# Performance work log

Hardware: AMD Instinct MI355X
Metric: run time of the kernel (lower is better)

Reference implementation:

```python
import jax, jax.numpy as jnp
import numpy as np

B, N, D, H = 4, 2048, 1024, 16
HD = D // H
LR_SCALE = 0.01  # base step size for the fast-weight test-time update
EPS = 1e-6


def setup_inputs() -> dict:
    key = jax.random.key(0)
    ks = jax.random.split(key, 11)
    s = 0.02
    x = jax.random.normal(ks[0], (B, N, D), jnp.float32)
    Wq = jax.random.normal(ks[1], (D, D), jnp.float32) * s
    Wk = jax.random.normal(ks[2], (D, D), jnp.float32) * s
    Wv = jax.random.normal(ks[3], (D, D), jnp.float32) * s
    Wo = jax.random.normal(ks[4], (D, D), jnp.float32) * s
    w1_init = jax.random.normal(ks[5], (H, HD, HD), jnp.float32) * s  # FastWeightGLU init state
    w3_init = jax.random.normal(ks[6], (H, HD, HD), jnp.float32) * s
    W_lr = jax.random.normal(ks[7], (D, H), jnp.float32) * s  # FastWeightHpGLU lr head
    norm_w = jnp.ones((D,), jnp.float32)  # grouped RMSNorm weight
    Wg1 = jax.random.normal(ks[8], (D, HD), jnp.float32) * s  # output_gate bottleneck
    Wg2 = jax.random.normal(ks[9], (HD, D), jnp.float32) * s
    return dict(x=x, Wq=Wq, Wk=Wk, Wv=Wv, Wo=Wo, w1_init=w1_init,
                w3_init=w3_init, W_lr=W_lr, norm_w=norm_w, Wg1=Wg1, Wg2=Wg2)


def _fast_weight_train(q, k, v, lr, w1_init, w3_init):
    # q,k,v: (b,n,h,hd); lr: (b,n,h); fast weight f(x) = silu(x@W1) * (x@W3)
    b = q.shape[0]
    W1_0 = jnp.broadcast_to(w1_init, (b,) + w1_init.shape)
    W3_0 = jnp.broadcast_to(w3_init, (b,) + w3_init.shape)

    def step(carry, inp):
        W1, W3 = carry
        q_t, k_t, v_t, lr_t = inp  # (b,h,hd), lr_t: (b,h,1)
        h1 = jnp.einsum('bhd,bhde->bhe', k_t, W1)
        h3 = jnp.einsum('bhd,bhde->bhe', k_t, W3)
        sg = jax.nn.sigmoid(h1)
        s1 = h1 * sg  # silu(h1)
        err = s1 * h3 - v_t  # d(0.5||f(k)-v||^2)/df
        dsilu = sg * (1.0 + h1 * (1.0 - sg))
        g1 = err * h3 * dsilu
        g3 = err * s1
        W1 = W1 - lr_t[..., None] * jnp.einsum('bhd,bhe->bhde', k_t, g1)
        W3 = W3 - lr_t[..., None] * jnp.einsum('bhd,bhe->bhde', k_t, g3)
        o1 = jnp.einsum('bhd,bhde->bhe', q_t, W1)
        o3 = jnp.einsum('bhd,bhde->bhe', q_t, W3)
        return (W1, W3), jax.nn.silu(o1) * o3

    xs = (q.transpose(1, 0, 2, 3), k.transpose(1, 0, 2, 3),
          v.transpose(1, 0, 2, 3), lr.transpose(1, 0, 2)[..., None])
    (W1, W3), outs = jax.lax.scan(step, (W1_0, W3_0), xs)
    return outs.transpose(1, 0, 2, 3), (W1, W3)  # (b,n,h,hd)


def reference(x, Wq, Wk, Wv, Wo, w1_init, w3_init, W_lr, norm_w, Wg1, Wg2):
    b, n, d = x.shape
    h = w1_init.shape[0]
    hd = d // h
    q = jax.nn.silu((x @ Wq).reshape(b, n, h, hd))
    k = jax.nn.silu((x @ Wk).reshape(b, n, h, hd))
    v = (x @ Wv).reshape(b, n, h, hd)
    lr = LR_SCALE * jax.nn.sigmoid(x @ W_lr)  # (b,n,h) per-token hyper-param
    out, _ = _fast_weight_train(q, k, v, lr, w1_init, w3_init)
    # grouped RMSNorm (per head) fused with sigmoid output gate
    rms = jax.lax.rsqrt(jnp.mean(out * out, axis=-1, keepdims=True) + EPS)
    out = (out * rms).reshape(b, n, d) * norm_w
    gate = (x @ Wg1) @ Wg2
    out = out * jax.nn.sigmoid(gate)
    return out @ Wo
```

## Files before the change

kernel.cpp:

```cpp
#include <hip/hip_runtime.h>
#include <hip/hip_bf16.h>

#define B_ 4
#define N_ 2048
#define D_ 1024
#define H_ 16
#define HD_ 64
#define MTOT (B_*N_)
#define CH_ 16
#define NCH_ (N_/CH_)

typedef __attribute__((ext_vector_type(8))) short short8v;
typedef __attribute__((ext_vector_type(4))) float f32x4;

__device__ __forceinline__ float fsig(float x){
  return __builtin_amdgcn_rcpf(1.0f + __expf(-x));
}

__global__ void k_cast_bf16(const float* __restrict__ in, __hip_bfloat16* __restrict__ out, int n4){
  int i = blockIdx.x*256 + threadIdx.x;
  if (i >= n4) return;
  float4 vv = ((const float4*)in)[i];
  __hip_bfloat16 b0 = __float2bfloat16(vv.x), b1 = __float2bfloat16(vv.y),
                 b2 = __float2bfloat16(vv.z), b3 = __float2bfloat16(vv.w);
  ushort4 o;
  o.x = *(const unsigned short*)&b0; o.y = *(const unsigned short*)&b1;
  o.z = *(const unsigned short*)&b2; o.w = *(const unsigned short*)&b3;
  ((ushort4*)out)[i] = o;
}

__global__ void k_transpose_cast(const float* __restrict__ in, __hip_bfloat16* __restrict__ out,
                                 int R, int C){
  __shared__ float tile[64][65];
  int r0 = blockIdx.y*64, c0 = blockIdx.x*64;
  int tid = threadIdx.x;
  #pragma unroll
  for (int i=0;i<16;i++){ int idx = tid + i*256; int rr = idx>>6, cc = idx&63;
    tile[rr][cc] = in[(size_t)(r0+rr)*C + (c0+cc)]; }
  __syncthreads();
  #pragma unroll
  for (int i=0;i<16;i++){ int idx = tid + i*256; int rr = idx>>6, cc = idx&63;
    out[(size_t)(c0+rr)*R + (r0+cc)] = __float2bfloat16(tile[cc][rr]); }
// ... 46 lines not shown
  short* lA = As + wid*1024;
  short* lB = Bs + wid*1024;
  const int row = lane & 15, kq = (lane >> 4)*8;
  for (int kk = 0; kk < K; kk += 32) {
    __syncthreads();
    gl2lds16(Aps + aoff0 + kk,                 lA);
    gl2lds16(Aps + aoff0 + (size_t)16*K + kk,  lA + 512);
    gl2lds16(Bps + boff0 + kk,                 lB);
    gl2lds16(Bps + boff0 + (size_t)16*K + kk,  lB + 512);
    __syncthreads();
    short8v af[4], bfr[4];
    #pragma unroll
    for (int i=0;i<4;i++) af[i]  = *(const short8v*)(As + (wm*64 + i*16 + row)*32 + kq);
    #pragma unroll
    for (int j=0;j<4;j++) bfr[j] = *(const short8v*)(Bs + (wn*64 + j*16 + row)*32 + kq);
    #pragma unroll
    for (int i=0;i<4;i++)
      #pragma unroll
      for (int j=0;j<4;j++)
        acc[i][j] = __builtin_amdgcn_mfma_f32_16x16x32_bf16(af[i], bfr[j], acc[i][j], 0, 0, 0);
  }
  #pragma unroll
  for (int i=0;i<4;i++){
    #pragma unroll
    for (int j=0;j<4;j++){
      int col = n0 + wn*64 + j*16 + (lane & 15);
      #pragma unroll
      for (int qq=0; qq<4; ++qq){
        int rowg = m0 + wm*64 + i*16 + (lane>>4)*4 + qq;
        float val = acc[i][j][qq];
        if (LAYOUT==0) {
          if (ACT==1) val = val*fsig(val);
          C[(size_t)rowg*N + col] = val;
        } else if (LAYOUT==1) {
          if (ACT==1) val = val*fsig(val);
          size_t oidx = ((((size_t)(rowg>>11))*16 + (col>>6))*(size_t)N_ + (size_t)(rowg & 2047))*64
                        + (size_t)(col & 63);
          C[oidx] = val;
        } else {
          const int t3 = col >> 10, cc2 = col & 1023;
          if (t3 < 2) val = val*fsig(val);
          size_t oidx = (size_t)t3*((size_t)MTOT*D_)
                      + ((((size_t)(rowg>>11))*16 + (cc2>>6))*(size_t)N_ + (size_t)(rowg & 2047))*64
                      + (size_t)(cc2 & 63);
          C[oidx] = val;
        }
      }
    }
  }
}

__device__ __forceinline__ unsigned short bfr16(float x){
  __hip_bfloat16 b = __float2bfloat16(x);
  return *(unsigned short*)&b;
}
__device__ __forceinline__ short8v cvt_frag(const float4 a, const float4 c){
  short8v r;
  r[0]=(short)bfr16(a.x); r[1]=(short)bfr16(a.y); r[2]=(short)bfr16(a.z); r[3]=(short)bfr16(a.w);
  r[4]=(short)bfr16(c.x); r[5]=(short)bfr16(c.y); r[6]=(short)bfr16(c.z); r[7]=(short)bfr16(c.w);
  return r;
}

__global__ __launch_bounds__(256,1) void k_scan8(
    const float* __restrict__ q, const float* __restrict__ k, const float* __restrict__ v,
    const float* __restrict__ lr, const float* __restrict__ w1i, const float* __restrict__ w3i,
    float* __restrict__ so)
{
  const int blk = blockIdx.x;
  const int bh  = blk >> 2;
  const int sl  = blk & 3;
  const int b = bh >> 4, h = bh & 15;
  const int e0 = sl*16;
  const int tid = threadIdx.x, lane = tid & 63, wid = tid >> 6;
  const int tA = lane & 15, ks8 = (lane >> 4)*8;

  __shared__ __align__(16) __hip_bfloat16 Wb1[16*64];
  __shared__ __align__(16) __hip_bfloat16 Wb3[16*64];
  __shared__ __align__(16) float KW1e[256], KW3e[256];
  __shared__ __align__(16) float QW1[256], QW3[256];
  __shared__ __align__(16) float GKK[256], GQK[256];
  __shared__ __align__(16) float C13[512];
  __shared__ __align__(16) float kS[16][68];

  const int we = tid & 15;
  const int wd = (tid >> 4) * 4;
  float w1r[4], w3r[4];
  {
    const float* w1p = w1i + (size_t)h*HD_*HD_ + e0 + we;
    const float* w3p = w3i + (size_t)h*HD_*HD_ + e0 + we;
    #pragma unroll
    for (int j=0;j<4;j++){ w1r[j] = w1p[(size_t)(wd+j)*64]; w3r[j] = w3p[(size_t)(wd+j)*64]; }
  }
  const int mir_off = we*128 + ((wd*2) ^ ((we&7)<<4));
  auto write_mirrors = [&](){
    uint2 p1, p3;
    p1.x = (unsigned)bfr16(w1r[0]) | ((unsigned)bfr16(w1r[1])<<16);
    p1.y = (unsigned)bfr16(w1r[2]) | ((unsigned)bfr16(w1r[3])<<16);
    p3.x = (unsigned)bfr16(w3r[0]) | ((unsigned)bfr16(w3r[1])<<16);
    p3.y = (unsigned)bfr16(w3r[2]) | ((unsigned)bfr16(w3r[3])<<16);
    *(uint2*)((char*)Wb1 + mir_off) = p1;
    *(uint2*)((char*)Wb3 + mir_off) = p3;
  };
  write_mirrors();

  const float* kfb = k + (size_t)bh*N_*64;
  const float* qfb = q + (size_t)bh*N_*64;
  const float* vfb = v + (size_t)bh*N_*64;
  const float* lrp = lr + ((size_t)b*N_)*16 + h;
  float* sob = so + (((size_t)b*N_)*16 + h)*64 + e0;

  auto mir_read = [&](const __hip_bfloat16* Wm, int m)->short8v{
    return *(const short8v*)((const char*)Wm + tA*128 + (((m*32+ks8)*2) ^ ((tA&7)<<4)));
  };

  float4 fA0,fA1,fA2,fA3;
  float4 fB0,fB1,fB2,fB3;
  float  vvr[16], lrr[16];

  if (wid >= 1) {
    const float* xr = ((wid==2) ? qfb : kfb) + (size_t)tA*64;
    fA0 = *(const float4*)(xr+ks8);    fA1 = *(const float4*)(xr+ks8+4);
    fA2 = *(const float4*)(xr+32+ks8); fA3 = *(const float4*)(xr+32+ks8+4);
    if (wid==3){
      const float* qr = qfb + (size_t)tA*64;
      fB0 = *(const float4*)(qr+ks8);    fB1 = *(const float4*)(qr+ks8+4);
      fB2 = *(const float4*)(qr+32+ks8); fB3 = *(const float4*)(qr+32+ks8+4);
    }
  } else if (lane < 16) {
    #pragma unroll
    for (int t=0;t<CH_;++t){
      vvr[t] = vfb[(size_t)t*64 + e0 + lane];
      lrr[t] = lrp[(size_t)t*16];
    }
  }
  __syncthreads();

  #pragma unroll 1
  for (int c = 0; c < NCH_; ++c) {
    const int t0 = c*CH_;

    if (wid == 1) {
      *(float4*)&kS[tA][ks8]      = fA0;
      *(float4*)&kS[tA][ks8+4]    = fA1;
      *(float4*)&kS[tA][32+ks8]   = fA2;
      *(float4*)&kS[tA][32+ks8+4] = fA3;
      short8v af0 = cvt_frag(fA0,fA1), af1 = cvt_frag(fA2,fA3);
      const int slot = (((lane>>4)*4) ^ ((( tA>>1)&3)<<2));
      f32x4 acc = {};
      acc = __builtin_amdgcn_mfma_f32_16x16x32_bf16(af0, mir_read(Wb1,0), acc, 0,0,0);
      acc = __builtin_amdgcn_mfma_f32_16x16x32_bf16(af1, mir_read(Wb1,1), acc, 0,0,0);
      *(f32x4*)&KW1e[tA*16 + slot] = acc;
      f32x4 ac3 = {};
      ac3 = __builtin_amdgcn_mfma_f32_16x16x32_bf16(af0, mir_read(Wb3,0), ac3, 0,0,0);
      ac3 = __builtin_amdgcn_mfma_f32_16x16x32_bf16(af1, mir_read(Wb3,1), ac3, 0,0,0);
      *(f32x4*)&KW3e[tA*16 + slot] = ac3;
    } else if (wid == 2) {
      short8v af0 = cvt_frag(fA0,fA1), af1 = cvt_frag(fA2,fA3);
      f32x4 acc = {};
      acc = __builtin_amdgcn_mfma_f32_16x16x32_bf16(af0, mir_read(Wb1,0), acc, 0,0,0);
      acc = __builtin_amdgcn_mfma_f32_16x16x32_bf16(af1, mir_read(Wb1,1), acc, 0,0,0);
      #pragma unroll
      for (int qq=0;qq<4;++qq) QW1[((lane>>4)*4+qq)*16 + tA] = acc[qq];
      f32x4 ac3 = {};
      ac3 = __builtin_amdgcn_mfma_f32_16x16x32_bf16(af0, mir_read(Wb3,0), ac3, 0,0,0);
      ac3 = __builtin_amdgcn_mfma_f32_16x16x32_bf16(af1, mir_read(Wb3,1), ac3, 0,0,0);
      #pragma unroll
      for (int qq=0;qq<4;++qq) QW3[((lane>>4)*4+qq)*16 + tA] = ac3[qq];
    } else if (wid == 3) {
      short8v af0 = cvt_frag(fA0,fA1), af1 = cvt_frag(fA2,fA3);
      short8v aq0 = cvt_frag(fB0,fB1), aq1 = cvt_frag(fB2,fB3);
      f32x4 acc = {};
      acc = __builtin_amdgcn_mfma_f32_16x16x32_bf16(af0, af0, acc, 0,0,0);
      acc = __builtin_amdgcn_mfma_f32_16x16x32_bf16(af1, af1, acc, 0,0,0);
      #pragma unroll
      for (int qq=0;qq<4;++qq) GKK[((lane>>4)*4+qq)*16 + tA] = acc[qq];
      f32x4 ac2 = {};
      ac2 = __builtin_amdgcn_mfma_f32_16x16x32_bf16(aq0, af0, ac2, 0,0,0);
      ac2 = __builtin_amdgcn_mfma_f32_16x16x32_bf16(aq1, af1, ac2, 0,0,0);
      #pragma unroll
      for (int qq=0;qq<4;++qq) GQK[((lane>>4)*4+qq)*16 + tA] = ac2[qq];
    }
    __syncthreads();

    const int tn0 = ((c+1 < NCH_) ? c+1 : c) * CH_;
    if (wid >= 1) {
      const float* xr = ((wid==2) ? qfb : kfb) + (size_t)(tn0+tA)*64;
      fA0 = *(const float4*)(xr+ks8);    fA1 = *(const float4*)(xr+ks8+4);
      fA2 = *(const float4*)(xr+32+ks8); fA3 = *(const float4*)(xr+32+ks8+4);
      if (wid==3){
        const float* qr = qfb + (size_t)(tn0+tA)*64;
        fB0 = *(const float4*)(qr+ks8);    fB1 = *(const float4*)(qr+ks8+4);
        fB2 = *(const float4*)(qr+32+ks8); fB3 = *(const float4*)(qr+32+ks8+4);
      }
    } else if (lane < 16) {
      float vvn[16], lrn[16];
      #pragma unroll
      for (int t=0;t<CH_;++t){
        vvn[t] = vfb[(size_t)(tn0+t)*64 + e0 + lane];
        lrn[t] = lrp[(size_t)(tn0+t)*16];
      }
      float a1[16], a3[16];
      const int swr = ((lane>>1)&3)<<2;
      #pragma unroll
      for (int i2=0;i2<4;i2++){
        f32x4 x1 = *(const f32x4*)&KW1e[lane*16 + ((i2*4) ^ swr)];
        f32x4 x3 = *(const f32x4*)&KW3e[lane*16 + ((i2*4) ^ swr)];
        a1[i2*4+0]=x1[0]; a1[i2*4+1]=x1[1]; a1[i2*4+2]=x1[2]; a1[i2*4+3]=x1[3];
        a3[i2*4+0]=x3[0]; a3[i2*4+1]=x3[1]; a3[i2*4+2]=x3[2]; a3[i2*4+3]=x3[3];
      }
      f32x4 grow[3][4];
      #pragma unroll
      for (int i2=0;i2<4;i2++){
        grow[0][i2] = *(const f32x4*)&GKK[ 0 + i2*4];
        grow[1][i2] = *(const f32x4*)&GKK[16 + i2*4];
        grow[2][i2] = *(const f32x4*)&GKK[32 + i2*4];
      }
      #pragma unroll
      for (int t = 0; t < CH_; ++t) {
        const float h1 = a1[t], h3 = a3[t];
        const float sg = fsig(h1);
        const float s1 = h1*sg;
        const float er = fmaf(s1, h3, -vvr[t]);
        const float ds = sg*fmaf(h1, 1.0f - sg, 1.0f);
        const float lt = lrr[t];
        float2 cc; cc.x = lt*(er*h3*ds); cc.y = lt*(er*s1);
        *(float2*)&C13[(t*16+lane)*2] = cc;
        #pragma unroll
        for (int t2 = t+1; t2 < CH_; ++t2) {
          const float g = grow[t%3][t2>>2][t2&3];
          a1[t2] = fmaf(-g, cc.x, a1[t2]);
          a3[t2] = fmaf(-g, cc.y, a3[t2]);
        }
        if (t + 3 < CH_) {
          #pragma unroll
          for (int i2=0;i2<4;i2++) grow[(t+3)%3][i2] = *(const f32x4*)&GKK[(t+3)*16 + i2*4];
        }
      }
      #pragma unroll
      for (int t=0;t<CH_;++t){ vvr[t]=vvn[t]; lrr[t]=lrn[t]; }
    }
    __syncthreads();

    {
      const int ot = tid >> 4, oe = tid & 15;
      float o1 = QW1[ot*16+oe], o3 = QW3[ot*16+oe];
      #pragma unroll
      for (int s = 0; s < CH_; ++s) {
        const float gl2 = GQK[ot*16+s];
        const float2 cc = *(const float2*)&C13[(s*16+oe)*2];
        const float g = (s <= ot) ? gl2 : 0.0f;
        o1 = fmaf(-g, cc.x, o1);
        o3 = fmaf(-g, cc.y, o3);
      }
      sob[(size_t)(t0+ot)*(H_*HD_) + oe] = (o1*fsig(o1))*o3;
    }

    #pragma unroll
    for (int s = 0; s < CH_; ++s) {
      const float2 cc = *(const float2*)&C13[(s*16+we)*2];
      const float4 ks = *(const float4*)&kS[s][wd];
      w1r[0] = fmaf(-ks.x, cc.x, w1r[0]); w1r[1] = fmaf(-ks.y, cc.x, w1r[1]);
      w1r[2] = fmaf(-ks.z, cc.x, w1r[2]); w1r[3] = fmaf(-ks.w, cc.x, w1r[3]);
      w3r[0] = fmaf(-ks.x, cc.y, w3r[0]); w3r[1] = fmaf(-ks.y, cc.y, w3r[1]);
      w3r[2] = fmaf(-ks.z, cc.y, w3r[2]); w3r[3] = fmaf(-ks.w, cc.y, w3r[3]);
    }
    write_mirrors();
    __syncthreads();
  }
}

__global__ void k_norm_gate(const float* __restrict__ so, const float* __restrict__ gate,
                            const float* __restrict__ nw, __hip_bfloat16* __restrict__ y)
{
  int idx = blockIdx.x*4 + (threadIdx.x>>6);
  int e = threadIdx.x & 63;
  float o = so[(size_t)idx*64 + e];
  float ss = o*o;
  #pragma unroll
  for (int m=32; m>=1; m>>=1) ss += __shfl_xor(ss, m, 64);
  float rms = rsqrtf(ss*(1.0f/64.0f) + 1e-6f);
  int hh = idx & 15;
  size_t bn = (size_t)(idx >> 4);
  int d = hh*64 + e;
  float g = gate[bn*1024 + d];
  float val = o*rms*nw[d] * fsig(g);
  y[bn*1024 + d] = __float2bfloat16(val);
}

extern "C" void kernel_launch(void* const* d_in, const int* in_sizes, int n_in,
                              void* d_out, int out_size, void* d_ws, size_t ws_size,
                              hipStream_t stream)
{
  const float* x   = (const float*)d_in[0];
  const float* Wq  = (const float*)d_in[1];
  const float* Wk  = (const float*)d_in[2];
  const float* Wv  = (const float*)d_in[3];
  const float* Wo  = (const float*)d_in[4];
  const float* w1i = (const float*)d_in[5];
  const float* w3i = (const float*)d_in[6];
  const float* Wlr = (const float*)d_in[7];
  const float* nw  = (const float*)d_in[8];
  const float* Wg1 = (const float*)d_in[9];
  const float* Wg2 = (const float*)d_in[10];
  float* out = (float*)d_out;

  char* p = (char*)d_ws;
  auto take = [&](size_t bytes)->void*{ void* r = (void*)p; p += (bytes + 255) & ~(size_t)255; return r; };
  __hip_bfloat16* xb    = (__hip_bfloat16*)take((size_t)MTOT*D_*2);
  __hip_bfloat16* WqkvT = (__hip_bfloat16*)take((size_t)3*D_*D_*2);
  __hip_bfloat16* Wot   = (__hip_bfloat16*)take((size_t)D_*D_*2);
  __hip_bfloat16* Wg2t  = (__hip_bfloat16*)take((size_t)D_*HD_*2);
  __hip_bfloat16* WgL   = (__hip_bfloat16*)take((size_t)128*D_*2);
  __hip_bfloat16* t1b   = (__hip_bfloat16*)take((size_t)MTOT*HD_*2);
  float* projt = (float*)take((size_t)MTOT*128*4);
  float* qf  = (float*)take((size_t)MTOT*D_*4);
  float* kf  = (float*)take((size_t)MTOT*D_*4);
  float* vf  = (float*)take((size_t)MTOT*D_*4);
  float* lrb = (float*)take((size_t)MTOT*H_*4);
  float* sob = (float*)take((size_t)MTOT*D_*4);
  __hip_bfloat16* yb = (__hip_bfloat16*)take((size_t)MTOT*D_*2);
  (void)kf; (void)vf;

  k_cast_bf16<<<MTOT*D_/4/256, 256, 0, stream>>>(x, xb, MTOT*D_/4);
  k_transpose_cast<<<dim3(16,16), 256, 0, stream>>>(Wq, WqkvT,             D_, D_);
  k_transpose_cast<<<dim3(16,16), 256, 0, stream>>>(Wk, WqkvT + D_*D_,     D_, D_);
  k_transpose_cast<<<dim3(16,16), 256, 0, stream>>>(Wv, WqkvT + 2*D_*D_,   D_, D_);
  k_transpose_cast<<<dim3(16,16), 256, 0, stream>>>(Wo, Wot, D_, D_);
  k_transpose_cast<<<dim3(16,1),  256, 0, stream>>>(Wg2, Wg2t, HD_, D_);
  k_prep_wgl<<<512, 256, 0, stream>>>(Wg1, Wlr, WgL);
  k_gemm_bt2<0,0><<<dim3(1,64), 256, 0, stream>>>(xb, WgL, projt, MTOT, 128, D_);
  k_post_gl<<<MTOT/4, 256, 0, stream>>>(projt, t1b, lrb);
  k_gemm_bt2<1,2><<<dim3(24,64), 256, 0, stream>>>(xb, WqkvT, qf, MTOT, 3*D_, D_);
  k_gemm_bt2<0,0><<<dim3(8,64), 256, 0, stream>>>(t1b, Wg2t, out, MTOT, D_, HD_);
  k_scan8<<<256, 256, 0, stream>>>(qf, kf, vf, lrb, w1i, w3i, sob);
  k_norm_gate<<<MTOT*H_/4, 256, 0, stream>>>(sob, out, nw, yb);
  k_gemm_bt2<0,0><<<dim3(8,64), 256, 0, stream>>>(yb, Wot, out, MTOT, D_, D_);
}
```

Measured before the change: 524.6 us.

## Double scan chunk size to 32 tokens and stage v/lr through shared memory

Raises the chunked fast-weight scan from 16 to 32 tokens per chunk, halving the number of serial chunk iterations and barriers, and extends the MFMA Gram/projection tiles to 32x32. v and lr prefetch moves from wave 0's registers to waves 1-3, which write them into shared memory after each chunk. The serial in-chunk recurrence on wave 0 grows quadratically with chunk size (32x32 triangle), and register pressure rises, which may offset the reduction in sync overhead.

```diff
diff --git a/kernel.cpp b/kernel.cpp
--- a/kernel.cpp
+++ b/kernel.cpp
@@ -7,7 +7,7 @@
 #define H_ 16
 #define HD_ 64
 #define MTOT (B_*N_)
-#define CH_ 16
+#define CH_ 32
 #define NCH_ (N_/CH_)
 
 typedef __attribute__((ext_vector_type(8))) short short8v;
@@ -149,7 +149,7 @@
   return r;
 }
 
-__global__ __launch_bounds__(256,1) void k_scan8(
+__global__ __launch_bounds__(256,1) void k_scan12(
     const float* __restrict__ q, const float* __restrict__ k, const float* __restrict__ v,
     const float* __restrict__ lr, const float* __restrict__ w1i, const float* __restrict__ w3i,
     float* __restrict__ so)
@@ -160,15 +160,18 @@
   const int b = bh >> 4, h = bh & 15;
   const int e0 = sl*16;
   const int tid = threadIdx.x, lane = tid & 63, wid = tid >> 6;
-  const int tA = lane & 15, ks8 = (lane >> 4)*8;
+  const int tA = lane & 15, g = lane >> 4;
+  const int ks8 = g*8;
 
   __shared__ __align__(16) __hip_bfloat16 Wb1[16*64];
   __shared__ __align__(16) __hip_bfloat16 Wb3[16*64];
-  __shared__ __align__(16) float KW1e[256], KW3e[256];
-  __shared__ __align__(16) float QW1[256], QW3[256];
-  __shared__ __align__(16) float GKK[256], GQK[256];
-  __shared__ __align__(16) float C13[512];
-  __shared__ __align__(16) float kS[16][68];
+  __shared__ __align__(16) float KW1e[16*32], KW3e[16*32];
+  __shared__ __align__(16) float QW1[32*16], QW3[32*16];
+  __shared__ __align__(16) float GKK[32*32], GQK[32*32];
+  __shared__ __align__(16) float C13[32*16*2];
+  __shared__ __align__(16) float kS[32][68];
+  __shared__ __align__(16) float vS[32*16];
+  __shared__ float lrS[32];
 
   const int we = tid & 15;
   const int wd = (tid >> 4) * 4;
@@ -201,26 +204,59 @@
     return *(const short8v*)((const char*)Wm + tA*128 + (((m*32+ks8)*2) ^ ((tA&7)<<4)));
   };
 
-  float4 fA0,fA1,fA2,fA3;
-  float4 fB0,fB1,fB2,fB3;
-  float  vvr[16], lrr[16];
-
-  if (wid >= 1) {
-    const float* xr = ((wid==2) ? qfb : kfb) + (size_t)tA*64;
-    fA0 = *(const float4*)(xr+ks8);    fA1 = *(const float4*)(xr+ks8+4);
-    fA2 = *(const float4*)(xr+32+ks8); fA3 = *(const float4*)(xr+32+ks8+4);
-    if (wid==3){
-      const float* qr = qfb + (size_t)tA*64;
-      fB0 = *(const float4*)(qr+ks8);    fB1 = *(const float4*)(qr+ks8+4);
-      fB2 = *(const float4*)(qr+32+ks8); fB3 = *(const float4*)(qr+32+ks8+4);
-    }
-  } else if (lane < 16) {
-    #pragma unroll
-    for (int t=0;t<CH_;++t){
-      vvr[t] = vfb[(size_t)t*64 + e0 + lane];
-      lrr[t] = lrp[(size_t)t*16];
-    }
-  }
+  float4 fK0,fK1,fK2,fK3,fK4,fK5,fK6,fK7;
+  float4 fQ0,fQ1,fQ2,fQ3,fQ4,fQ5,fQ6,fQ7;
+  float  vPr0,vPr1,vPr2,vPr3;
+  float  lrPr = 0.f;
+
+  auto load_kq = [&](int t0n){
+    if (wid==1 || wid==3){
+      const float* kr0 = kfb + (size_t)(t0n+tA)*64;
+      const float* kr1 = kfb + (size_t)(t0n+16+tA)*64;
+      fK0 = *(const float4*)(kr0+ks8);    fK1 = *(const float4*)(kr0+ks8+4);
+      fK2 = *(const float4*)(kr0+32+ks8); fK3 = *(const float4*)(kr0+32+ks8+4);
+      fK4 = *(const float4*)(kr1+ks8);    fK5 = *(const float4*)(kr1+ks8+4);
+      fK6 = *(const float4*)(kr1+32+ks8); fK7 = *(const float4*)(kr1+32+ks8+4);
+    }
+    if (wid==2 || wid==3){
+      const float* qr0 = qfb + (size_t)(t0n+tA)*64;
+      const float* qr1 = qfb + (size_t)(t0n+16+tA)*64;
+      fQ0 = *(const float4*)(qr0+ks8);    fQ1 = *(const float4*)(qr0+ks8+4);
+      fQ2 = *(const float4*)(qr0+32+ks8); fQ3 = *(const float4*)(qr0+32+ks8+4);
+      fQ4 = *(const float4*)(qr1+ks8);    fQ5 = *(const float4*)(qr1+ks8+4);
+      fQ6 = *(const float4*)(qr1+32+ks8); fQ7 = *(const float4*)(qr1+32+ks8+4);
+    }
+    if (wid==1){
+      #pragma unroll
+      for (int i=0;i<4;i++){
+        int idx = lane + 64*i;
+        ((float*)&vPr0)[0];
+      }
+      vPr0 = vfb[(size_t)(t0n + ((lane+  0)>>4))*64 + e0 + ((lane+  0)&15)];
+      vPr1 = vfb[(size_t)(t0n + ((lane+ 64)>>4))*64 + e0 + ((lane+ 64)&15)];
+      vPr2 = vfb[(size_t)(t0n + ((lane+128)>>4))*64 + e0 + ((lane+128)&15)];
+      vPr3 = vfb[(size_t)(t0n + ((lane+192)>>4))*64 + e0 + ((lane+192)&15)];
+    } else if (wid==2){
+      vPr0 = vfb[(size_t)(t0n + 16 + ((lane+  0)>>4))*64 + e0 + ((lane+  0)&15)];
+      vPr1 = vfb[(size_t)(t0n + 16 + ((lane+ 64)>>4))*64 + e0 + ((lane+ 64)&15)];
+      vPr2 = vfb[(size_t)(t0n + 16 + ((lane+128)>>4))*64 + e0 + ((lane+128)&15)];
+      vPr3 = vfb[(size_t)(t0n + 16 + ((lane+192)>>4))*64 + e0 + ((lane+192)&15)];
+    } else if (wid==3 && lane<32){
+      lrPr = lrp[(size_t)(t0n+lane)*16];
+    }
+  };
+  auto store_vlr = [&](){
+    if (wid==1){
+      vS[lane+  0] = vPr0; vS[lane+ 64] = vPr1; vS[lane+128] = vPr2; vS[lane+192] = vPr3;
+    } else if (wid==2){
+      vS[256+lane+  0] = vPr0; vS[256+lane+ 64] = vPr1; vS[256+lane+128] = vPr2; vS[256+lane+192] = vPr3;
+    } else if (wid==3 && lane<32){
+      lrS[lane] = lrPr;
+    }
+  };
+
+  load_kq(0);
+  store_vlr();
   __syncthreads();
 
   #pragma unroll 1
@@ -228,119 +264,165 @@
     const int t0 = c*CH_;
 
     if (wid == 1) {
-      *(float4*)&kS[tA][ks8]      = fA0;
-      *(float4*)&kS[tA][ks8+4]    = fA1;
-      *(float4*)&kS[tA][32+ks8]   = fA2;
-      *(float4*)&kS[tA][32+ks8+4] = fA3;
-      short8v af0 = cvt_frag(fA0,fA1), af1 = cvt_frag(fA2,fA3);
-      const int slot = (((lane>>4)*4) ^ ((( tA>>1)&3)<<2));
+      *(float4*)&kS[tA][ks8]         = fK0;  *(float4*)&kS[tA][ks8+4]       = fK1;
+      *(float4*)&kS[tA][32+ks8]      = fK2;  *(float4*)&kS[tA][32+ks8+4]    = fK3;
+      *(float4*)&kS[16+tA][ks8]      = fK4;  *(float4*)&kS[16+tA][ks8+4]    = fK5;
+      *(float4*)&kS[16+tA][32+ks8]   = fK6;  *(float4*)&kS[16+tA][32+ks8+4] = fK7;
+      short8v a0 = cvt_frag(fK0,fK1), a1f = cvt_frag(fK2,fK3);
+      short8v b0 = cvt_frag(fK4,fK5), b1f = cvt_frag(fK6,fK7);
+      const int slot = (g*4) ^ (((tA>>1)&3)<<2);
       f32x4 acc = {};
-      acc = __builtin_amdgcn_mfma_f32_16x16x32_bf16(af0, mir_read(Wb1,0), acc, 0,0,0);
-      acc = __builtin_amdgcn_mfma_f32_16x16x32_bf16(af1, mir_read(Wb1,1), acc, 0,0,0);
-      *(f32x4*)&KW1e[tA*16 + slot] = acc;
+      acc = __builtin_amdgcn_mfma_f32_16x16x32_bf16(a0, mir_read(Wb1,0), acc, 0,0,0);
+      acc = __builtin_amdgcn_mfma_f32_16x16x32_bf16(a1f, mir_read(Wb1,1), acc, 0,0,0);
+      *(f32x4*)&KW1e[tA*32 + slot] = acc;
+      f32x4 ac2 = {};
+      ac2 = __builtin_amdgcn_mfma_f32_16x16x32_bf16(b0, mir_read(Wb1,0), ac2, 0,0,0);
+      ac2 = __builtin_amdgcn_mfma_f32_16x16x32_bf16(b1f, mir_read(Wb1,1), ac2, 0,0,0);
+      *(f32x4*)&KW1e[tA*32 + 16 + slot] = ac2;
       f32x4 ac3 = {};
-      ac3 = __builtin_amdgcn_mfma_f32_16x16x32_bf16(af0, mir_read(Wb3,0), ac3, 0,0,0);
-      ac3 = __builtin_amdgcn_mfma_f32_16x16x32_bf16(af1, mir_read(Wb3,1), ac3, 0,0,0);
-      *(f32x4*)&KW3e[tA*16 + slot] = ac3;
+      ac3 = __builtin_amdgcn_mfma_f32_16x16x32_bf16(a0, mir_read(Wb3,0), ac3, 0,0,0);
+      ac3 = __builtin_amdgcn_mfma_f32_16x16x32_bf16(a1f, mir_read(Wb3,1), ac3, 0,0,0);
+      *(f32x4*)&KW3e[tA*32 + slot] = ac3;
+      f32x4 ac4 = {};
+      ac4 = __builtin_amdgcn_mfma_f32_16x16x32_bf16(b0, mir_read(Wb3,0), ac4, 0,0,0);
+      ac4 = __builtin_amdgcn_mfma_f32_16x16x32_bf16(b1f, mir_read(Wb3,1), ac4, 0,0,0);
+      *(f32x4*)&KW3e[tA*32 + 16 + slot] = ac4;
     } else if (wid == 2) {
-      short8v af0 = cvt_frag(fA0,fA1), af1 = cvt_frag(fA2,fA3);
+      short8v a0 = cvt_frag(fQ0,fQ1), a1f = cvt_frag(fQ2,fQ3);
+      short8v b0 = cvt_frag(fQ4,fQ5), b1f = cvt_frag(fQ6,fQ7);
       f32x4 acc = {};
-      acc = __builtin_amdgcn_mfma_f32_16x16x32_bf16(af0, mir_read(Wb1,0), acc, 0,0,0);
-      acc = __builtin_amdgcn_mfma_f32_16x16x32_bf16(af1, mir_read(Wb1,1), acc, 0,0,0);
-      #pragma unroll
-      for (int qq=0;qq<4;++qq) QW1[((lane>>4)*4+qq)*16 + tA] = acc[qq];
+      acc = __builtin_amdgcn_mfma_f32_16x16x32_bf16(a0, mir_read(Wb1,0), acc, 0,0,0);
+      acc = __builtin_amdgcn_mfma_f32_16x16x32_bf16(a1f, mir_read(Wb1,1), acc, 0,0,0);
+      #pragma unroll
+      for (int qq=0;qq<4;++qq) QW1[(g*4+qq)*16 + tA] = acc[qq];
+      f32x4 ac2 = {};
+      ac2 = __builtin_amdgcn_mfma_f32_16x16x32_bf16(b0, mir_read(Wb1,0), ac2, 0,0,0);
+      ac2 = __builtin_amdgcn_mfma_f32_16x16x32_bf16(b1f, mir_read(Wb1,1), ac2, 0,0,0);
+      #pragma unroll
+      for (int qq=0;qq<4;++qq) QW1[(16+g*4+qq)*16 + tA] = ac2[qq];
       f32x4 ac3 = {};
-      ac3 = __builtin_amdgcn_mfma_f32_16x16x32_bf16(af0, mir_read(Wb3,0), ac3, 0,0,0);
-      ac3 = __builtin_amdgcn_mfma_f32_16x16x32_bf16(af1, mir_read(Wb3,1), ac3, 0,0,0);
-      #pragma unroll
-      for (int qq=0;qq<4;++qq) QW3[((lane>>4)*4+qq)*16 + tA] = ac3[qq];
+      ac3 = __builtin_amdgcn_mfma_f32_16x16x32_bf16(a0, mir_read(Wb3,0), ac3, 0,0,0);
+      ac3 = __builtin_amdgcn_mfma_f32_16x16x32_bf16(a1f, mir_read(Wb3,1), ac3, 0,0,0);
+      #pragma unroll
+      for (int qq=0;qq<4;++qq) QW3[(g*4+qq)*16 + tA] = ac3[qq];
+      f32x4 ac4 = {};
+      ac4 = __builtin_amdgcn_mfma_f32_16x16x32_bf16(b0, mir_read(Wb3,0), ac4, 0,0,0);
+      ac4 = __builtin_amdgcn_mfma_f32_16x16x32_bf16(b1f, mir_read(Wb3,1), ac4, 0,0,0);
+      #pragma unroll
+      for (int qq=0;qq<4;++qq) QW3[(16+g*4+qq)*16 + tA] = ac4[qq];
     } else if (wid == 3) {
-      short8v af0 = cvt_frag(fA0,fA1), af1 = cvt_frag(fA2,fA3);
-      short8v aq0 = cvt_frag(fB0,fB1), aq1 = cvt_frag(fB2,fB3);
-      f32x4 acc = {};
-      acc = __builtin_amdgcn_mfma_f32_16x16x32_bf16(af0, af0, acc, 0,0,0);
-      acc = __builtin_amdgcn_mfma_f32_16x16x32_bf16(af1, af1, acc, 0,0,0);
-      #pragma unroll
-      for (int qq=0;qq<4;++qq) GKK[((lane>>4)*4+qq)*16 + tA] = acc[qq];
-      f32x4 ac2 = {};
-      ac2 = __builtin_amdgcn_mfma_f32_16x16x32_bf16(aq0, af0, ac2, 0,0,0);
-      ac2 = __builtin_amdgcn_mfma_f32_16x16x32_bf16(aq1, af1, ac2, 0,0,0);
-      #pragma unroll
-      for (int qq=0;qq<4;++qq) GQK[((lane>>4)*4+qq)*16 + tA] = ac2[qq];
+      short8v ka0 = cvt_frag(fK0,fK1), ka1 = cvt_frag(fK2,fK3);
+      short8v kb0 = cvt_frag(fK4,fK5), kb1 = cvt_frag(fK6,fK7);
+      short8v qa0 = cvt_frag(fQ0,fQ1), qa1 = cvt_frag(fQ2,fQ3);
+      short8v qb0 = cvt_frag(fQ4,fQ5), qb1 = cvt_frag(fQ6,fQ7);
+      {
+        f32x4 t00 = {}, t01 = {}, t10 = {}, t11 = {};
+        t00 = __builtin_amdgcn_mfma_f32_16x16x32_bf16(ka0, ka0, t00, 0,0,0);
+        t00 = __builtin_amdgcn_mfma_f32_16x16x32_bf16(ka1, ka1, t00, 0,0,0);
+        t01 = __builtin_amdgcn_mfma_f32_16x16x32_bf16(ka0, kb0, t01, 0,0,0);
+        t01 = __builtin_amdgcn_mfma_f32_16x16x32_bf16(ka1, kb1, t01, 0,0,0);
+        t10 = __builtin_amdgcn_mfma_f32_16x16x32_bf16(kb0, ka0, t10, 0,0,0);
+        t10 = __builtin_amdgcn_mfma_f32_16x16x32_bf16(kb1, ka1, t10, 0,0,0);
+        t11 = __builtin_amdgcn_mfma_f32_16x16x32_bf16(kb0, kb0, t11, 0,0,0);
+        t11 = __builtin_amdgcn_mfma_f32_16x16x32_bf16(kb1, kb1, t11, 0,0,0);
+        #pragma unroll
+        for (int qq=0;qq<4;++qq){
+          GKK[(g*4+qq)*32 + tA]        = t00[qq];
+          GKK[(g*4+qq)*32 + 16 + tA]   = t01[qq];
+          GKK[(16+g*4+qq)*32 + tA]     = t10[qq];
+          GKK[(16+g*4+qq)*32 + 16+tA]  = t11[qq];
+        }
+      }
+      {
+        f32x4 u00 = {}, u10 = {}, u11 = {};
+        u00 = __builtin_amdgcn_mfma_f32_16x16x32_bf16(qa0, ka0, u00, 0,0,0);
+        u00 = __builtin_amdgcn_mfma_f32_16x16x32_bf16(qa1, ka1, u00, 0,0,0);
+        u10 = __builtin_amdgcn_mfma_f32_16x16x32_bf16(qb0, ka0, u10, 0,0,0);
+        u10 = __builtin_amdgcn_mfma_f32_16x16x32_bf16(qb1, ka1, u10, 0,0,0);
+        u11 = __builtin_amdgcn_mfma_f32_16x16x32_bf16(qb0, kb0, u11, 0,0,0);
+        u11 = __builtin_amdgcn_mfma_f32_16x16x32_bf16(qb1, kb1, u11, 0,0,0);
+        #pragma unroll
+        for (int qq=0;qq<4;++qq){
+          GQK[(g*4+qq)*32 + tA]        = u00[qq];
+          GQK[(16+g*4+qq)*32 + tA]     = u10[qq];
+          GQK[(16+g*4+qq)*32 + 16+tA]  = u11[qq];
+        }
+      }
     }
     __syncthreads();
 
     const int tn0 = ((c+1 < NCH_) ? c+1 : c) * CH_;
     if (wid >= 1) {
-      const float* xr = ((wid==2) ? qfb : kfb) + (size_t)(tn0+tA)*64;
-      fA0 = *(const float4*)(xr+ks8);    fA1 = *(const float4*)(xr+ks8+4);
-      fA2 = *(const float4*)(xr+32+ks8); fA3 = *(const float4*)(xr+32+ks8+4);
-      if (wid==3){
-        const float* qr = qfb + (size_t)(tn0+tA)*64;
-        fB0 = *(const float4*)(qr+ks8);    fB1 = *(const float4*)(qr+ks8+4);
-        fB2 = *(const float4*)(qr+32+ks8); fB3 = *(const float4*)(qr+32+ks8+4);
-      }
+      load_kq(tn0);
     } else if (lane < 16) {
-      float vvn[16], lrn[16];
-      #pragma unroll
-      for (int t=0;t<CH_;++t){
-        vvn[t] = vfb[(size_t)(tn0+t)*64 + e0 + lane];
-        lrn[t] = lrp[(size_t)(tn0+t)*16];
-      }
-      float a1[16], a3[16];
+      float a1[32], a3[32];
       const int swr = ((lane>>1)&3)<<2;
       #pragma unroll
-      for (int i2=0;i2<4;i2++){
-        f32x4 x1 = *(const f32x4*)&KW1e[lane*16 + ((i2*4) ^ swr)];
-        f32x4 x3 = *(const f32x4*)&KW3e[lane*16 + ((i2*4) ^ swr)];
-        a1[i2*4+0]=x1[0]; a1[i2*4+1]=x1[1]; a1[i2*4+2]=x1[2]; a1[i2*4+3]=x1[3];
-        a3[i2*4+0]=x3[0]; a3[i2*4+1]=x3[1]; a3[i2*4+2]=x3[2]; a3[i2*4+3]=x3[3];
-      }
-      f32x4 grow[3][4];
-      #pragma unroll
-      for (int i2=0;i2<4;i2++){
+      for (int X=0;X<2;X++)
+        #pragma unroll
+        for (int i2=0;i2<4;i2++){
+          f32x4 x1 = *(const f32x4*)&KW1e[lane*32 + X*16 + ((i2*4) ^ swr)];
+          f32x4 x3 = *(const f32x4*)&KW3e[lane*32 + X*16 + ((i2*4) ^ swr)];
+          a1[X*16+i2*4+0]=x1[0]; a1[X*16+i2*4+1]=x1[1]; a1[X*16+i2*4+2]=x1[2]; a1[X*16+i2*4+3]=x1[3];
+          a3[X*16+i2*4+0]=x3[0]; a3[X*16+i2*4+1]=x3[1]; a3[X*16+i2*4+2]=x3[2]; a3[X*16+i2*4+3]=x3[3];
+        }
+      f32x4 grow[3][8];
+      #pragma unroll
+      for (int i2=0;i2<8;i2++){
         grow[0][i2] = *(const f32x4*)&GKK[ 0 + i2*4];
-        grow[1][i2] = *(const f32x4*)&GKK[16 + i2*4];
-        grow[2][i2] = *(const f32x4*)&GKK[32 + i2*4];
+        grow[1][i2] = *(const f32x4*)&GKK[32 + i2*4];
+        grow[2][i2] = *(const f32x4*)&GKK[64 + i2*4];
       }
       #pragma unroll
       for (int t = 0; t < CH_; ++t) {
         const float h1 = a1[t], h3 = a3[t];
         const float sg = fsig(h1);
         const float s1 = h1*sg;
-        const float er = fmaf(s1, h3, -vvr[t]);
+        const float er = fmaf(s1, h3, -vS[t*16+lane]);
         const float ds = sg*fmaf(h1, 1.0f - sg, 1.0f);
-        const float lt = lrr[t];
+        const float lt = lrS[t];
         float2 cc; cc.x = lt*(er*h3*ds); cc.y = lt*(er*s1);
         *(float2*)&C13[(t*16+lane)*2] = cc;
         #pragma unroll
         for (int t2 = t+1; t2 < CH_; ++t2) {
-          const float g = grow[t%3][t2>>2][t2&3];
-          a1[t2] = fmaf(-g, cc.x, a1[t2]);
-          a3[t2] = fmaf(-g, cc.y, a3[t2]);
+          const float gg = grow[t%3][t2>>2][t2&3];
+          a1[t2] = fmaf(-gg, cc.x, a1[t2]);
+          a3[t2] = fmaf(-gg, cc.y, a3[t2]);
         }
         if (t + 3 < CH_) {
           #pragma unroll
-          for (int i2=0;i2<4;i2++) grow[(t+3)%3][i2] = *(const f32x4*)&GKK[(t+3)*16 + i2*4];
-        }
-      }
-      #pragma unroll
-      for (int t=0;t<CH_;++t){ vvr[t]=vvn[t]; lrr[t]=lrn[t]; }
+          for (int i2=0;i2<8;i2++) grow[(t+3)%3][i2] = *(const f32x4*)&GKK[(t+3)*32 + i2*4];
+        }
+      }
     }
     __syncthreads();
 
     {
-      const int ot = tid >> 4, oe = tid & 15;
-      float o1 = QW1[ot*16+oe], o3 = QW3[ot*16+oe];
-      #pragma unroll
-      for (int s = 0; s < CH_; ++s) {
-        const float gl2 = GQK[ot*16+s];
-        const float2 cc = *(const float2*)&C13[(s*16+oe)*2];
-        const float g = (s <= ot) ? gl2 : 0.0f;
-        o1 = fmaf(-g, cc.x, o1);
-        o3 = fmaf(-g, cc.y, o3);
-      }
-      sob[(size_t)(t0+ot)*(H_*HD_) + oe] = (o1*fsig(o1))*o3;
+      const int oe = tid & 15, otb = tid >> 4;
+      float c1r[32], c3r[32];
+      #pragma unroll
+      for (int s=0;s<CH_;++s){
+        float2 cc = *(const float2*)&C13[(s*16+oe)*2];
+        c1r[s]=cc.x; c3r[s]=cc.y;
+      }
+      #pragma unroll
+      for (int pr=0; pr<2; ++pr){
+        const int ot = otb + pr*16;
+        float o1 = QW1[ot*16+oe], o3 = QW3[ot*16+oe];
+        float gq[32];
+        #pragma unroll
+        for (int i2=0;i2<8;i2++){
+          f32x4 a = *(const f32x4*)&GQK[ot*32 + i2*4];
+          gq[i2*4]=a[0]; gq[i2*4+1]=a[1]; gq[i2*4+2]=a[2]; gq[i2*4+3]=a[3];
+        }
+        #pragma unroll
+        for (int s=0;s<CH_;++s){
+          const float gg = (s <= ot) ? gq[s] : 0.0f;
+          o1 = fmaf(-gg, c1r[s], o1);
+          o3 = fmaf(-gg, c3r[s], o3);
+        }
+        sob[(size_t)(t0+ot)*(H_*HD_) + oe] = (o1*fsig(o1))*o3;
+      }
     }
 
     #pragma unroll
@@ -353,6 +435,7 @@
       w3r[2] = fmaf(-ks.z, cc.y, w3r[2]); w3r[3] = fmaf(-ks.w, cc.y, w3r[3]);
     }
     write_mirrors();
+    store_vlr();
     __syncthreads();
   }
 }
@@ -420,7 +503,7 @@
   k_post_gl<<<MTOT/4, 256, 0, stream>>>(projt, t1b, lrb);
   k_gemm_bt2<1,2><<<dim3(24,64), 256, 0, stream>>>(xb, WqkvT, qf, MTOT, 3*D_, D_);
   k_gemm_bt2<0,0><<<dim3(8,64), 256, 0, stream>>>(t1b, Wg2t, out, MTOT, D_, HD_);
-  k_scan8<<<256, 256, 0, stream>>>(qf, kf, vf, lrb, w1i, w3i, sob);
+  k_scan12<<<256, 256, 0, stream>>>(qf, kf, vf, lrb, w1i, w3i, sob);
   k_norm_gate<<<MTOT*H_/4, 256, 0, stream>>>(sob, out, nw, yb);
   k_gemm_bt2<0,0><<<dim3(8,64), 256, 0, stream>>>(yb, Wot, out, MTOT, D_, D_);
 }
```

Result: slower. 570.4 us (+8.7%).

## Store QKV as bf16 and defer scan output computation to overlap next chunk

Applied to the files above, without the earlier changes.

The QKV projection GEMM now writes bf16 instead of fp32, halving its store traffic and the scan kernel's load traffic, and the scan reads bf16 fragments directly into MFMA without a conversion step. Inside the scan, the per-chunk output computation is delayed by one chunk and run on waves 1-3 while wave 0 does the serial gradient recurrence. Double-buffered shared arrays (QW, GQK, C13) make this possible, which removes one serial phase from the critical path of each chunk. The cost is lower precision for q, k and v (rounded to bf16 before the fp32 weight update) and more shared memory.

```diff
diff --git a/kernel.cpp b/kernel.cpp
--- a/kernel.cpp
+++ b/kernel.cpp
@@ -120,18 +120,13 @@
         if (LAYOUT==0) {
           if (ACT==1) val = val*fsig(val);
           C[(size_t)rowg*N + col] = val;
-        } else if (LAYOUT==1) {
-          if (ACT==1) val = val*fsig(val);
-          size_t oidx = ((((size_t)(rowg>>11))*16 + (col>>6))*(size_t)N_ + (size_t)(rowg & 2047))*64
-                        + (size_t)(col & 63);
-          C[oidx] = val;
         } else {
           const int t3 = col >> 10, cc2 = col & 1023;
           if (t3 < 2) val = val*fsig(val);
           size_t oidx = (size_t)t3*((size_t)MTOT*D_)
                       + ((((size_t)(rowg>>11))*16 + (cc2>>6))*(size_t)N_ + (size_t)(rowg & 2047))*64
                       + (size_t)(cc2 & 63);
-          C[oidx] = val;
+          ((__hip_bfloat16*)C)[oidx] = __float2bfloat16(val);
         }
       }
     }
@@ -142,16 +137,11 @@
   __hip_bfloat16 b = __float2bfloat16(x);
   return *(unsigned short*)&b;
 }
-__device__ __forceinline__ short8v cvt_frag(const float4 a, const float4 c){
-  short8v r;
-  r[0]=(short)bfr16(a.x); r[1]=(short)bfr16(a.y); r[2]=(short)bfr16(a.z); r[3]=(short)bfr16(a.w);
-  r[4]=(short)bfr16(c.x); r[5]=(short)bfr16(c.y); r[6]=(short)bfr16(c.z); r[7]=(short)bfr16(c.w);
-  return r;
-}
-
-__global__ __launch_bounds__(256,1) void k_scan8(
-    const float* __restrict__ q, const float* __restrict__ k, const float* __restrict__ v,
-    const float* __restrict__ lr, const float* __restrict__ w1i, const float* __restrict__ w3i,
+
+__global__ __launch_bounds__(256,1) void k_scan13(
+    const __hip_bfloat16* __restrict__ q, const __hip_bfloat16* __restrict__ k,
+    const __hip_bfloat16* __restrict__ v, const float* __restrict__ lr,
+    const float* __restrict__ w1i, const float* __restrict__ w3i,
     float* __restrict__ so)
 {
   const int blk = blockIdx.x;
@@ -165,9 +155,10 @@
   __shared__ __align__(16) __hip_bfloat16 Wb1[16*64];
   __shared__ __align__(16) __hip_bfloat16 Wb3[16*64];
   __shared__ __align__(16) float KW1e[256], KW3e[256];
-  __shared__ __align__(16) float QW1[256], QW3[256];
-  __shared__ __align__(16) float GKK[256], GQK[256];
-  __shared__ __align__(16) float C13[512];
+  __shared__ __align__(16) float QW1[2][256], QW3[2][256];
+  __shared__ __align__(16) float GKK[256];
+  __shared__ __align__(16) float GQK[2][256];
+  __shared__ __align__(16) float C13[2][512];
   __shared__ __align__(16) float kS[16][68];
 
   const int we = tid & 15;
@@ -191,9 +182,9 @@
   };
   write_mirrors();
 
-  const float* kfb = k + (size_t)bh*N_*64;
-  const float* qfb = q + (size_t)bh*N_*64;
-  const float* vfb = v + (size_t)bh*N_*64;
+  const short* kps = (const short*)(k + (size_t)bh*N_*64);
+  const short* qps = (const short*)(q + (size_t)bh*N_*64);
+  const __hip_bfloat16* vfb = v + (size_t)bh*N_*64;
   const float* lrp = lr + ((size_t)b*N_)*16 + h;
   float* sob = so + (((size_t)b*N_)*16 + h)*64 + e0;
 
@@ -201,23 +192,22 @@
     return *(const short8v*)((const char*)Wm + tA*128 + (((m*32+ks8)*2) ^ ((tA&7)<<4)));
   };
 
-  float4 fA0,fA1,fA2,fA3;
-  float4 fB0,fB1,fB2,fB3;
+  short8v pK0, pK1;
+  short8v pQ0, pQ1;
   float  vvr[16], lrr[16];
 
-  if (wid >= 1) {
-    const float* xr = ((wid==2) ? qfb : kfb) + (size_t)tA*64;
-    fA0 = *(const float4*)(xr+ks8);    fA1 = *(const float4*)(xr+ks8+4);
-    fA2 = *(const float4*)(xr+32+ks8); fA3 = *(const float4*)(xr+32+ks8+4);
-    if (wid==3){
-      const float* qr = qfb + (size_t)tA*64;
-      fB0 = *(const float4*)(qr+ks8);    fB1 = *(const float4*)(qr+ks8+4);
-      fB2 = *(const float4*)(qr+32+ks8); fB3 = *(const float4*)(qr+32+ks8+4);
-    }
-  } else if (lane < 16) {
+  if (wid==1 || wid==3){
+    pK0 = *(const short8v*)(kps + (size_t)tA*64 + ks8);
+    pK1 = *(const short8v*)(kps + (size_t)tA*64 + 32 + ks8);
+  }
+  if (wid==2 || wid==3){
+    pQ0 = *(const short8v*)(qps + (size_t)tA*64 + ks8);
+    pQ1 = *(const short8v*)(qps + (size_t)tA*64 + 32 + ks8);
+  }
+  if (wid==0 && lane < 16) {
     #pragma unroll
     for (int t=0;t<CH_;++t){
-      vvr[t] = vfb[(size_t)t*64 + e0 + lane];
+      vvr[t] = __bfloat162float(vfb[(size_t)t*64 + e0 + lane]);
       lrr[t] = lrp[(size_t)t*16];
     }
   }
@@ -226,65 +216,97 @@
   #pragma unroll 1
   for (int c = 0; c < NCH_; ++c) {
     const int t0 = c*CH_;
+    const int par = c & 1;
 
     if (wid == 1) {
-      *(float4*)&kS[tA][ks8]      = fA0;
-      *(float4*)&kS[tA][ks8+4]    = fA1;
-      *(float4*)&kS[tA][32+ks8]   = fA2;
-      *(float4*)&kS[tA][32+ks8+4] = fA3;
-      short8v af0 = cvt_frag(fA0,fA1), af1 = cvt_frag(fA2,fA3);
-      const int slot = (((lane>>4)*4) ^ ((( tA>>1)&3)<<2));
+      float kf_[16];
+      #pragma unroll
+      for (int j=0;j<4;j++){
+        unsigned u = ((const unsigned*)&pK0)[j];
+        kf_[2*j]   = __uint_as_float(u << 16);
+        kf_[2*j+1] = __uint_as_float(u & 0xffff0000u);
+      }
+      #pragma unroll
+      for (int j=0;j<4;j++){
+        unsigned u = ((const unsigned*)&pK1)[j];
+        kf_[8+2*j]   = __uint_as_float(u << 16);
+        kf_[8+2*j+1] = __uint_as_float(u & 0xffff0000u);
+      }
+      f32x4 s0 = {kf_[0],kf_[1],kf_[2],kf_[3]};   *(f32x4*)&kS[tA][ks8]      = s0;
+      f32x4 s1 = {kf_[4],kf_[5],kf_[6],kf_[7]};   *(f32x4*)&kS[tA][ks8+4]    = s1;
+      f32x4 s2 = {kf_[8],kf_[9],kf_[10],kf_[11]}; *(f32x4*)&kS[tA][32+ks8]   = s2;
+      f32x4 s3 = {kf_[12],kf_[13],kf_[14],kf_[15]};*(f32x4*)&kS[tA][32+ks8+4]= s3;
+      const int slot = (((lane>>4)*4) ^ (((tA>>1)&3)<<2));
       f32x4 acc = {};
-      acc = __builtin_amdgcn_mfma_f32_16x16x32_bf16(af0, mir_read(Wb1,0), acc, 0,0,0);
-      acc = __builtin_amdgcn_mfma_f32_16x16x32_bf16(af1, mir_read(Wb1,1), acc, 0,0,0);
+      acc = __builtin_amdgcn_mfma_f32_16x16x32_bf16(pK0, mir_read(Wb1,0), acc, 0,0,0);
+      acc = __builtin_amdgcn_mfma_f32_16x16x32_bf16(pK1, mir_read(Wb1,1), acc, 0,0,0);
       *(f32x4*)&KW1e[tA*16 + slot] = acc;
       f32x4 ac3 = {};
-      ac3 = __builtin_amdgcn_mfma_f32_16x16x32_bf16(af0, mir_read(Wb3,0), ac3, 0,0,0);
-      ac3 = __builtin_amdgcn_mfma_f32_16x16x32_bf16(af1, mir_read(Wb3,1), ac3, 0,0,0);
+      ac3 = __builtin_amdgcn_mfma_f32_16x16x32_bf16(pK0, mir_read(Wb3,0), ac3, 0,0,0);
+      ac3 = __builtin_amdgcn_mfma_f32_16x16x32_bf16(pK1, mir_read(Wb3,1), ac3, 0,0,0);
       *(f32x4*)&KW3e[tA*16 + slot] = ac3;
     } else if (wid == 2) {
-      short8v af0 = cvt_frag(fA0,fA1), af1 = cvt_frag(fA2,fA3);
       f32x4 acc = {};
-      acc = __builtin_amdgcn_mfma_f32_16x16x32_bf16(af0, mir_read(Wb1,0), acc, 0,0,0);
-      acc = __builtin_amdgcn_mfma_f32_16x16x32_bf16(af1, mir_read(Wb1,1), acc, 0,0,0);
-      #pragma unroll
-      for (int qq=0;qq<4;++qq) QW1[((lane>>4)*4+qq)*16 + tA] = acc[qq];
+      acc = __builtin_amdgcn_mfma_f32_16x16x32_bf16(pQ0, mir_read(Wb1,0), acc, 0,0,0);
+      acc = __builtin_amdgcn_mfma_f32_16x16x32_bf16(pQ1, mir_read(Wb1,1), acc, 0,0,0);
+      #pragma unroll
+      for (int qq=0;qq<4;++qq) QW1[par][((lane>>4)*4+qq)*16 + tA] = acc[qq];
       f32x4 ac3 = {};
-      ac3 = __builtin_amdgcn_mfma_f32_16x16x32_bf16(af0, mir_read(Wb3,0), ac3, 0,0,0);
-      ac3 = __builtin_amdgcn_mfma_f32_16x16x32_bf16(af1, mir_read(Wb3,1), ac3, 0,0,0);
-      #pragma unroll
-      for (int qq=0;qq<4;++qq) QW3[((lane>>4)*4+qq)*16 + tA] = ac3[qq];
+      ac3 = __builtin_amdgcn_mfma_f32_16x16x32_bf16(pQ0, mir_read(Wb3,0), ac3, 0,0,0);
+      ac3 = __builtin_amdgcn_mfma_f32_16x16x32_bf16(pQ1, mir_read(Wb3,1), ac3, 0,0,0);
+      #pragma unroll
+      for (int qq=0;qq<4;++qq) QW3[par][((lane>>4)*4+qq)*16 + tA] = ac3[qq];
     } else if (wid == 3) {
-      short8v af0 = cvt_frag(fA0,fA1), af1 = cvt_frag(fA2,fA3);
-      short8v aq0 = cvt_frag(fB0,fB1), aq1 = cvt_frag(fB2,fB3);
       f32x4 acc = {};
-      acc = __builtin_amdgcn_mfma_f32_16x16x32_bf16(af0, af0, acc, 0,0,0);
-      acc = __builtin_amdgcn_mfma_f32_16x16x32_bf16(af1, af1, acc, 0,0,0);
+      acc = __builtin_amdgcn_mfma_f32_16x16x32_bf16(pK0, pK0, acc, 0,0,0);
+      acc = __builtin_amdgcn_mfma_f32_16x16x32_bf16(pK1, pK1, acc, 0,0,0);
       #pragma unroll
       for (int qq=0;qq<4;++qq) GKK[((lane>>4)*4+qq)*16 + tA] = acc[qq];
       f32x4 ac2 = {};
-      ac2 = __builtin_amdgcn_mfma_f32_16x16x32_bf16(aq0, af0, ac2, 0,0,0);
-      ac2 = __builtin_amdgcn_mfma_f32_16x16x32_bf16(aq1, af1, ac2, 0,0,0);
-      #pragma unroll
-      for (int qq=0;qq<4;++qq) GQK[((lane>>4)*4+qq)*16 + tA] = ac2[qq];
+      ac2 = __builtin_amdgcn_mfma_f32_16x16x32_bf16(pQ0, pK0, ac2, 0,0,0);
+      ac2 = __builtin_amdgcn_mfma_f32_16x16x32_bf16(pQ1, pK1, ac2, 0,0,0);
+      #pragma unroll
+      for (int qq=0;qq<4;++qq) GQK[par][((lane>>4)*4+qq)*16 + tA] = ac2[qq];
     }
     __syncthreads();
 
     const int tn0 = ((c+1 < NCH_) ? c+1 : c) * CH_;
     if (wid >= 1) {
-      const float* xr = ((wid==2) ? qfb : kfb) + (size_t)(tn0+tA)*64;
-      fA0 = *(const float4*)(xr+ks8);    fA1 = *(const float4*)(xr+ks8+4);
-      fA2 = *(const float4*)(xr+32+ks8); fA3 = *(const float4*)(xr+32+ks8+4);
-      if (wid==3){
-        const float* qr = qfb + (size_t)(tn0+tA)*64;
-        fB0 = *(const float4*)(qr+ks8);    fB1 = *(const float4*)(qr+ks8+4);
-        fB2 = *(const float4*)(qr+32+ks8); fB3 = *(const float4*)(qr+32+ks8+4);
+      if (wid==1 || wid==3){
+        pK0 = *(const short8v*)(kps + (size_t)(tn0+tA)*64 + ks8);
+        pK1 = *(const short8v*)(kps + (size_t)(tn0+tA)*64 + 32 + ks8);
+      }
+      if (wid==2 || wid==3){
+        pQ0 = *(const short8v*)(qps + (size_t)(tn0+tA)*64 + ks8);
+        pQ1 = *(const short8v*)(qps + (size_t)(tn0+tA)*64 + 32 + ks8);
+      }
+      if (c > 0) {
+        const int parp = par ^ 1;
+        const int bt = t0 - CH_;
+        const int p0 = tid - 64;
+        #pragma unroll
+        for (int rep=0; rep<2; ++rep){
+          const int pp = p0 + rep*192;
+          if (pp < 256){
+            const int ot = pp >> 4, oe = pp & 15;
+            float o1 = QW1[parp][ot*16+oe], o3 = QW3[parp][ot*16+oe];
+            #pragma unroll
+            for (int s = 0; s < CH_; ++s) {
+              const float gl2 = GQK[parp][ot*16+s];
+              const float2 cc = *(const float2*)&C13[parp][(s*16+oe)*2];
+              const float g = (s <= ot) ? gl2 : 0.0f;
+              o1 = fmaf(-g, cc.x, o1);
+              o3 = fmaf(-g, cc.y, o3);
+            }
+            sob[(size_t)(bt+ot)*(H_*HD_) + oe] = (o1*fsig(o1))*o3;
+          }
+        }
       }
     } else if (lane < 16) {
       float vvn[16], lrn[16];
       #pragma unroll
       for (int t=0;t<CH_;++t){
-        vvn[t] = vfb[(size_t)(tn0+t)*64 + e0 + lane];
+        vvn[t] = __bfloat162float(vfb[(size_t)(tn0+t)*64 + e0 + lane]);
         lrn[t] = lrp[(size_t)(tn0+t)*16];
       }
       float a1[16], a3[16];
@@ -312,7 +334,7 @@
         const float ds = sg*fmaf(h1, 1.0f - sg, 1.0f);
         const float lt = lrr[t];
         float2 cc; cc.x = lt*(er*h3*ds); cc.y = lt*(er*s1);
-        *(float2*)&C13[(t*16+lane)*2] = cc;
+        *(float2*)&C13[par][(t*16+lane)*2] = cc;
         #pragma unroll
         for (int t2 = t+1; t2 < CH_; ++t2) {
           const float g = grow[t%3][t2>>2][t2&3];
@@ -329,23 +351,9 @@
     }
     __syncthreads();
 
-    {
-      const int ot = tid >> 4, oe = tid & 15;
-      float o1 = QW1[ot*16+oe], o3 = QW3[ot*16+oe];
-      #pragma unroll
-      for (int s = 0; s < CH_; ++s) {
-        const float gl2 = GQK[ot*16+s];
-        const float2 cc = *(const float2*)&C13[(s*16+oe)*2];
-        const float g = (s <= ot) ? gl2 : 0.0f;
-        o1 = fmaf(-g, cc.x, o1);
-        o3 = fmaf(-g, cc.y, o3);
-      }
-      sob[(size_t)(t0+ot)*(H_*HD_) + oe] = (o1*fsig(o1))*o3;
-    }
-
     #pragma unroll
     for (int s = 0; s < CH_; ++s) {
-      const float2 cc = *(const float2*)&C13[(s*16+we)*2];
+      const float2 cc = *(const float2*)&C13[par][(s*16+we)*2];
       const float4 ks = *(const float4*)&kS[s][wd];
       w1r[0] = fmaf(-ks.x, cc.x, w1r[0]); w1r[1] = fmaf(-ks.y, cc.x, w1r[1]);
       w1r[2] = fmaf(-ks.z, cc.x, w1r[2]); w1r[3] = fmaf(-ks.w, cc.x, w1r[3]);
@@ -354,6 +362,29 @@
     }
     write_mirrors();
     __syncthreads();
+  }
+
+  if (wid >= 1) {
+    const int parp = (NCH_-1) & 1;
+    const int bt = (NCH_-1)*CH_;
+    const int p0 = tid - 64;
+    #pragma unroll
+    for (int rep=0; rep<2; ++rep){
+      const int pp = p0 + rep*192;
+      if (pp < 256){
+        const int ot = pp >> 4, oe = pp & 15;
+        float o1 = QW1[parp][ot*16+oe], o3 = QW3[parp][ot*16+oe];
+        #pragma unroll
+        for (int s = 0; s < CH_; ++s) {
+          const float gl2 = GQK[parp][ot*16+s];
+          const float2 cc = *(const float2*)&C13[parp][(s*16+oe)*2];
+          const float g = (s <= ot) ? gl2 : 0.0f;
+          o1 = fmaf(-g, cc.x, o1);
+          o3 = fmaf(-g, cc.y, o3);
+        }
+        sob[(size_t)(bt+ot)*(H_*HD_) + oe] = (o1*fsig(o1))*o3;
+      }
+    }
   }
 }
 
@@ -401,13 +432,12 @@
   __hip_bfloat16* WgL   = (__hip_bfloat16*)take((size_t)128*D_*2);
   __hip_bfloat16* t1b   = (__hip_bfloat16*)take((size_t)MTOT*HD_*2);
   float* projt = (float*)take((size_t)MTOT*128*4);
-  float* qf  = (float*)take((size_t)MTOT*D_*4);
-  float* kf  = (float*)take((size_t)MTOT*D_*4);
-  float* vf  = (float*)take((size_t)MTOT*D_*4);
+  __hip_bfloat16* qb = (__hip_bfloat16*)take((size_t)MTOT*D_*2);
+  __hip_bfloat16* kb = (__hip_bfloat16*)take((size_t)MTOT*D_*2);
+  __hip_bfloat16* vb = (__hip_bfloat16*)take((size_t)MTOT*D_*2);
   float* lrb = (float*)take((size_t)MTOT*H_*4);
   float* sob = (float*)take((size_t)MTOT*D_*4);
   __hip_bfloat16* yb = (__hip_bfloat16*)take((size_t)MTOT*D_*2);
-  (void)kf; (void)vf;
 
   k_cast_bf16<<<MTOT*D_/4/256, 256, 0, stream>>>(x, xb, MTOT*D_/4);
   k_transpose_cast<<<dim3(16,16), 256, 0, stream>>>(Wq, WqkvT,             D_, D_);
@@ -418,9 +448,9 @@
   k_prep_wgl<<<512, 256, 0, stream>>>(Wg1, Wlr, WgL);
   k_gemm_bt2<0,0><<<dim3(1,64), 256, 0, stream>>>(xb, WgL, projt, MTOT, 128, D_);
   k_post_gl<<<MTOT/4, 256, 0, stream>>>(projt, t1b, lrb);
-  k_gemm_bt2<1,2><<<dim3(24,64), 256, 0, stream>>>(xb, WqkvT, qf, MTOT, 3*D_, D_);
+  k_gemm_bt2<1,2><<<dim3(24,64), 256, 0, stream>>>(xb, WqkvT, (float*)qb, MTOT, 3*D_, D_);
   k_gemm_bt2<0,0><<<dim3(8,64), 256, 0, stream>>>(t1b, Wg2t, out, MTOT, D_, HD_);
-  k_scan8<<<256, 256, 0, stream>>>(qf, kf, vf, lrb, w1i, w3i, sob);
+  k_scan13<<<256, 256, 0, stream>>>(qb, kb, vb, lrb, w1i, w3i, sob);
   k_norm_gate<<<MTOT*H_/4, 256, 0, stream>>>(sob, out, nw, yb);
   k_gemm_bt2<0,0><<<dim3(8,64), 256, 0, stream>>>(yb, Wot, out, MTOT, D_, D_);
 }
```

New measurement: 497.7 us. 5.1% less time.
